# Kernel optimization log

Hardware: AMD Instinct MI355X
Metric: run time of the kernel (lower is better)

The kernel has to match this reference:

```python
import jax, jax.numpy as jnp
import numpy as np

IN_FEATURES = 1024
OUT_FEATURES = 64
DEGREE = 3
NUM_KNOTS = 10
BATCH = 8192
K0 = NUM_KNOTS + DEGREE  # number of basis columns / control points per edge


def b_spline_basis(x, knots, degree):
    """Vectorized Cox-de Boor recursion.
    x: (..., ) values in [0,1]; knots: (K0+1,).
    Returns (..., K0) basis; last `degree` columns are zero-padded (matches
    control_points width of num_knots+degree as in the original module).
    """
    t = knots
    n0 = t.shape[0] - 1  # = K0 degree-0 intervals
    xe = x[..., None]
    basis = ((xe >= t[:-1]) & (xe < t[1:])).astype(x.dtype)  # (..., K0)
    for p in range(1, degree + 1):
        ti = t[: n0 - p]
        tip = t[p:n0]
        ti1 = t[1 : n0 - p + 1]
        tip1 = t[p + 1 : n0 + 1]
        d1 = jnp.where(tip - ti > 0, tip - ti, jnp.ones_like(ti))
        d2 = jnp.where(tip1 - ti1 > 0, tip1 - ti1, jnp.ones_like(ti1))
        left = jnp.where(tip - ti > 0, (xe - ti) / d1, 0.0) * basis[..., : n0 - p]
        right = jnp.where(tip1 - ti1 > 0, (tip1 - xe) / d2, 0.0) * basis[..., 1 : n0 - p + 1]
        new = left + right
        pad = jnp.zeros(x.shape + (p,), x.dtype)
        basis = jnp.concatenate([new, pad], axis=-1)
    return basis


def setup_inputs() -> dict:
    key = jax.random.key(0)
    k1, k2 = jax.random.split(key)
    x = jax.random.uniform(k1, (BATCH, IN_FEATURES), dtype=jnp.float32)
    knots = jnp.linspace(0.0, 1.0, NUM_KNOTS + DEGREE + 1, dtype=jnp.float32)
    control_points = jax.random.normal(k2, (OUT_FEATURES, IN_FEATURES, K0), dtype=jnp.float32)
    return {"x": x, "knots": knots, "control_points": control_points}


def reference(x, knots, control_points):
    # basis: (B, in, K0) computed once per input feature (original recomputes
    # it out_features times inside a double loop -- same math, fused here).
    basis = b_spline_basis(x, knots, DEGREE)
    # outputs[b, o] = sum_j sum_k basis[b, j, k] * control_points[o, j, k]
    return jnp.einsum("bjk,ojk->bo", basis, control_points)
```

## Files before the change

kernel.cpp:

```cpp
#include <hip/hip_runtime.h>
#include <hip/hip_bf16.h>
#include <stdint.h>

#define IN_F   1024
#define OUT_F  64
#define BATCH  8192
#define BM     128
#define JSPLIT 16
#define JPB    (IN_F / JSPLIT)
#define JC     8
#define NCH    (JPB / JC)
#define BT_BYTES  (JC * 2048)
#define X_BYTES   (BM * JC * 4)
#define BUF_BYTES (BT_BYTES + X_BYTES)
#define OUTSZ  (BATCH * OUT_F)

typedef __attribute__((ext_vector_type(8)))  short short8;
typedef __attribute__((ext_vector_type(16))) float f32x16;

__global__ void kan_prep(const float* __restrict__ cp, __hip_bfloat16* __restrict__ bt) {
    int j = blockIdx.x * 4 + (threadIdx.x >> 6);
    int o = threadIdx.x & 63;
    const float* src = cp + ((size_t)o * IN_F + j) * 13;
    float v[16];
#pragma unroll
    for (int k = 0; k < 13; ++k) v[k] = src[k];
#pragma unroll
    for (int k = 13; k < 16; ++k) v[k] = 0.0f;
    __hip_bfloat16* dst = bt + (size_t)j * 1024;
#pragma unroll
    for (int kh = 0; kh < 2; ++kh)
#pragma unroll
        for (int e = 0; e < 8; ++e)
            dst[kh * 512 + o * 8 + e] = __float2bfloat16(v[kh * 8 + e]);
}

__device__ __forceinline__ uint64_t funnel64(uint64_t V, int p) {
    uint64_t r;
    if (p >= 0) r = (p >= 64) ? 0ull : (V << p);
    else { int q = -p; r = (q >= 64) ? 0ull : (V >> q); }
    return r;
}

template<bool PART>
__launch_bounds__(256, 4)
__global__ void kan_main(const float* __restrict__ x,
                         const __hip_bfloat16* __restrict__ bt,
                         float* __restrict__ outp) {
    __shared__ __attribute__((aligned(16))) char lds[2 * BUF_BYTES];

    const int tid   = threadIdx.x;
    const int w     = tid >> 6;
    const int lane  = tid & 63;
    const int l31   = lane & 31;
    const int khalf = lane >> 5;
    const int k0    = khalf << 3;

    const int r0 = blockIdx.x * BM;
    const int j0 = blockIdx.y * JPB;

    const char*  btg = (const char*)bt + (size_t)j0 * 2048;
    const float* xg  = x + (size_t)(r0 + (tid >> 1)) * IN_F + j0 + (tid & 1) * 4;

    uint4 g0, g1, g2, g3, gx;

#define LOAD(ch) do {                                            \
        const char* cb = btg + (ch) * BT_BYTES + tid * 16;       \
        g0 = *(const uint4*)(cb);                                \
        g1 = *(const uint4*)(cb + 4096);                         \
        g2 = *(const uint4*)(cb + 8192);                         \
        g3 = *(const uint4*)(cb + 12288);                        \
        gx = *(const uint4*)(xg + (ch) * JC);                    \
    } while (0)

#define WRITE(boff) do {                                         \
        char* d = lds + (boff) + tid * 16;                       \
        *(uint4*)(d)          = g0;                              \
        *(uint4*)(d + 4096)   = g1;                              \
        *(uint4*)(d + 8192)   = g2;                              \
        *(uint4*)(d + 12288)  = g3;                              \
        *(uint4*)(lds + (boff) + BT_BYTES + tid * 16) = gx;      \
    } while (0)

    f32x16 acc0, acc1;
#pragma unroll
    for (int i = 0; i < 16; ++i) { acc0[i] = 0.0f; acc1[i] = 0.0f; }

    LOAD(0);
    WRITE(0);
    LOAD(1);
    __syncthreads();

    int cur = 0;
#pragma unroll 1
    for (int ch = 0; ch < NCH; ++ch) {
        if (ch + 1 < NCH) WRITE(cur ^ BUF_BYTES);
        if (ch + 2 < NCH) LOAD(ch + 2);

        {
            const char* base = lds + cur;
            float xv[8];
            const char* xr = base + BT_BYTES + (w * 32 + l31) * 32;
            *(float4*)&xv[0] = *(const float4*)(xr);
            *(float4*)&xv[4] = *(const float4*)(xr + 16);
            const char* bbb = base + khalf * 1024 + l31 * 16;
#pragma unroll
            for (int jl = 0; jl < JC; ++jl) {
                const short8 b0 = *(const short8*)(bbb + jl * 2048);
                const short8 b1 = *(const short8*)(bbb + jl * 2048 + 512);

                const float xvv = xv[jl];
                float t  = xvv * 13.0f;
                float mf = floorf(t);
                mf = fminf(mf, 12.0f);
                float uu = t - mf;
                int   m  = (int)mf;
                float u2 = uu * uu, u3 = u2 * uu;
                float B3 = u3 * (1.0f / 6.0f);
                float omu = 1.0f - uu;
                float B0 = omu * omu * omu * (1.0f / 6.0f);
                float B1 = (0.5f * u3 - u2) + (2.0f / 3.0f);
                float B2 = 1.0f - B0 - B1 - B3;
                B3 = (m >= 10) ? 0.0f : B3;
                B2 = (m >= 11) ? 0.0f : B2;
                B1 = (m >= 12) ? 0.0f : B1;
                uint32_t P01, P23;
                asm("v_cvt_pk_bf16_f32 %0, %1, %2" : "=v"(P01) : "v"(B0), "v"(B1));
                asm("v_cvt_pk_bf16_f32 %0, %1, %2" : "=v"(P23) : "v"(B2), "v"(B3));
                uint64_t V = ((uint64_t)P23 << 32) | (uint64_t)P01;
                int p = ((m - 3 - k0) << 4);
                uint64_t flo = funnel64(V, p);
                uint64_t fhi = funnel64(V, p - 64);
                union { uint64_t q[2]; short8 s; } cv;
                cv.q[0] = flo; cv.q[1] = fhi;

                acc0 = __builtin_amdgcn_mfma_f32_32x32x16_bf16(cv.s, b0, acc0, 0, 0, 0);
                acc1 = __builtin_amdgcn_mfma_f32_32x32x16_bf16(cv.s, b1, acc1, 0, 0, 0);
            }
        }

        if (ch + 1 < NCH) __syncthreads();
        cur ^= BUF_BYTES;
    }
#undef LOAD
#undef WRITE

    float* op = PART ? (outp + (size_t)blockIdx.y * OUTSZ) : outp;
#pragma unroll
    for (int r = 0; r < 16; ++r) {
        int row = (r & 3) + 8 * (r >> 2) + 4 * khalf;
        float* po = op + (size_t)(r0 + w * 32 + row) * OUT_F;
        if (PART) {
            po[l31]      = acc0[r];
            po[l31 + 32] = acc1[r];
        } else {
            atomicAdd(po + l31,      acc0[r]);
            atomicAdd(po + l31 + 32, acc1[r]);
        }
    }
}

__global__ void kan_reduce(const float* __restrict__ part, float* __restrict__ out) {
    const int i = (blockIdx.x * 256 + threadIdx.x) * 4;
    float4 s = {0.0f, 0.0f, 0.0f, 0.0f};
#pragma unroll
    for (int b = 0; b < JSPLIT; ++b) {
        const float4 v = *(const float4*)(part + (size_t)b * OUTSZ + i);
        s.x += v.x; s.y += v.y; s.z += v.z; s.w += v.w;
    }
    *(float4*)(out + i) = s;
}

extern "C" void kernel_launch(void* const* d_in, const int* in_sizes, int n_in,
                              void* d_out, int out_size, void* d_ws, size_t ws_size,
                              hipStream_t stream) {
    const float* x  = (const float*)d_in[0];
    const float* cp = (const float*)d_in[2];
    float* out = (float*)d_out;
    __hip_bfloat16* bt = (__hip_bfloat16*)d_ws;
    float* part = (float*)((char*)d_ws + 2 * 1024 * 1024);

    const size_t need = 2u * 1024u * 1024u + (size_t)JSPLIT * OUTSZ * 4u;
    const bool use_part = ws_size >= need;

    kan_prep<<<dim3(IN_F / 4), dim3(256), 0, stream>>>(cp, bt);
    if (use_part) {
        kan_main<true><<<dim3(BATCH / BM, JSPLIT), dim3(256), 0, stream>>>(x, bt, part);
        kan_reduce<<<dim3(OUTSZ / 1024), dim3(256), 0, stream>>>(part, out);
    } else {
        hipMemsetAsync(d_out, 0, (size_t)out_size * sizeof(float), stream);
        kan_main<false><<<dim3(BATCH / BM, JSPLIT), dim3(256), 0, stream>>>(x, bt, out);
    }
}
```

Before: 49.30 us.

## Double the J-split, halve chunk size, and store bf16 partial sums

Raises the split of the input-feature dimension from 16 to 32 blocks and halves the per-chunk width to 4, with launch bounds raised to 8 blocks per CU, to get more blocks in flight and more occupancy. Partial outputs are now written as bf16 instead of fp32, which halves partial-buffer traffic, and the reduce kernel widens to 8 elements per thread with bf16-to-fp32 conversion. The cost is twice as many partial buffers for the reduce to read, shorter pipelines per block, and lower precision in the partial sums.

```diff
diff --git a/kernel.cpp b/kernel.cpp
--- a/kernel.cpp
+++ b/kernel.cpp
@@ -6,9 +6,9 @@
 #define OUT_F  64
 #define BATCH  8192
 #define BM     128
-#define JSPLIT 16
+#define JSPLIT 32
 #define JPB    (IN_F / JSPLIT)
-#define JC     8
+#define JC     4
 #define NCH    (JPB / JC)
 #define BT_BYTES  (JC * 2048)
 #define X_BYTES   (BM * JC * 4)
@@ -43,10 +43,10 @@
 }
 
 template<bool PART>
-__launch_bounds__(256, 4)
+__launch_bounds__(256, 8)
 __global__ void kan_main(const float* __restrict__ x,
                          const __hip_bfloat16* __restrict__ bt,
-                         float* __restrict__ outp) {
+                         void* __restrict__ outp) {
     __shared__ __attribute__((aligned(16))) char lds[2 * BUF_BYTES];
 
     const int tid   = threadIdx.x;
@@ -60,26 +60,23 @@
     const int j0 = blockIdx.y * JPB;
 
     const char*  btg = (const char*)bt + (size_t)j0 * 2048;
-    const float* xg  = x + (size_t)(r0 + (tid >> 1)) * IN_F + j0 + (tid & 1) * 4;
-
-    uint4 g0, g1, g2, g3, gx;
+    const float* xg  = x + (size_t)(r0 + (tid >> 1)) * IN_F + j0 + (tid & 1) * 2;
+
+    uint4  g0, g1;
+    float2 gx;
 
 #define LOAD(ch) do {                                            \
-        const char* cb = btg + (ch) * BT_BYTES + tid * 16;       \
+        const char* cb = btg + (ch) * BT_BYTES + tid * 32;       \
         g0 = *(const uint4*)(cb);                                \
-        g1 = *(const uint4*)(cb + 4096);                         \
-        g2 = *(const uint4*)(cb + 8192);                         \
-        g3 = *(const uint4*)(cb + 12288);                        \
-        gx = *(const uint4*)(xg + (ch) * JC);                    \
+        g1 = *(const uint4*)(cb + 16);                           \
+        gx = *(const float2*)(xg + (ch) * JC);                   \
     } while (0)
 
 #define WRITE(boff) do {                                         \
-        char* d = lds + (boff) + tid * 16;                       \
-        *(uint4*)(d)          = g0;                              \
-        *(uint4*)(d + 4096)   = g1;                              \
-        *(uint4*)(d + 8192)   = g2;                              \
-        *(uint4*)(d + 12288)  = g3;                              \
-        *(uint4*)(lds + (boff) + BT_BYTES + tid * 16) = gx;      \
+        char* d = lds + (boff) + tid * 32;                       \
+        *(uint4*)(d)      = g0;                                  \
+        *(uint4*)(d + 16) = g1;                                  \
+        *(float2*)(lds + (boff) + BT_BYTES + tid * 8) = gx;      \
     } while (0)
 
     f32x16 acc0, acc1;
@@ -99,10 +96,8 @@
 
         {
             const char* base = lds + cur;
-            float xv[8];
-            const char* xr = base + BT_BYTES + (w * 32 + l31) * 32;
-            *(float4*)&xv[0] = *(const float4*)(xr);
-            *(float4*)&xv[4] = *(const float4*)(xr + 16);
+            float xv[4];
+            *(float4*)&xv[0] = *(const float4*)(base + BT_BYTES + (w * 32 + l31) * 16);
             const char* bbb = base + khalf * 1024 + l31 * 16;
 #pragma unroll
             for (int jl = 0; jl < JC; ++jl) {
@@ -145,30 +140,44 @@
 #undef LOAD
 #undef WRITE
 
-    float* op = PART ? (outp + (size_t)blockIdx.y * OUTSZ) : outp;
-#pragma unroll
-    for (int r = 0; r < 16; ++r) {
-        int row = (r & 3) + 8 * (r >> 2) + 4 * khalf;
-        float* po = op + (size_t)(r0 + w * 32 + row) * OUT_F;
-        if (PART) {
-            po[l31]      = acc0[r];
-            po[l31 + 32] = acc1[r];
-        } else {
+    if (PART) {
+        __hip_bfloat16* op = (__hip_bfloat16*)outp + (size_t)blockIdx.y * OUTSZ;
+#pragma unroll
+        for (int r = 0; r < 16; ++r) {
+            int row = (r & 3) + 8 * (r >> 2) + 4 * khalf;
+            __hip_bfloat16* po = op + (size_t)(r0 + w * 32 + row) * OUT_F;
+            po[l31]      = __float2bfloat16(acc0[r]);
+            po[l31 + 32] = __float2bfloat16(acc1[r]);
+        }
+    } else {
+        float* op = (float*)outp;
+#pragma unroll
+        for (int r = 0; r < 16; ++r) {
+            int row = (r & 3) + 8 * (r >> 2) + 4 * khalf;
+            float* po = op + (size_t)(r0 + w * 32 + row) * OUT_F;
             atomicAdd(po + l31,      acc0[r]);
             atomicAdd(po + l31 + 32, acc1[r]);
         }
     }
 }
 
-__global__ void kan_reduce(const float* __restrict__ part, float* __restrict__ out) {
-    const int i = (blockIdx.x * 256 + threadIdx.x) * 4;
-    float4 s = {0.0f, 0.0f, 0.0f, 0.0f};
+__global__ void kan_reduce(const __hip_bfloat16* __restrict__ part,
+                           float* __restrict__ out) {
+    const int i = (blockIdx.x * 256 + threadIdx.x) * 8;
+    float s[8] = {0, 0, 0, 0, 0, 0, 0, 0};
 #pragma unroll
     for (int b = 0; b < JSPLIT; ++b) {
-        const float4 v = *(const float4*)(part + (size_t)b * OUTSZ + i);
-        s.x += v.x; s.y += v.y; s.z += v.z; s.w += v.w;
-    }
-    *(float4*)(out + i) = s;
+        const short8 v = *(const short8*)(part + (size_t)b * OUTSZ + i);
+#pragma unroll
+        for (int e = 0; e < 8; ++e) {
+            union { uint32_t u; float f; } c;
+            c.u = ((uint32_t)(uint16_t)v[e]) << 16;
+            s[e] += c.f;
+        }
+    }
+    float4 lo = {s[0], s[1], s[2], s[3]}, hi = {s[4], s[5], s[6], s[7]};
+    *(float4*)(out + i)     = lo;
+    *(float4*)(out + i + 4) = hi;
 }
 
 extern "C" void kernel_launch(void* const* d_in, const int* in_sizes, int n_in,
@@ -177,18 +186,18 @@
     const float* x  = (const float*)d_in[0];
     const float* cp = (const float*)d_in[2];
     float* out = (float*)d_out;
-    __hip_bfloat16* bt = (__hip_bfloat16*)d_ws;
-    float* part = (float*)((char*)d_ws + 2 * 1024 * 1024);
-
-    const size_t need = 2u * 1024u * 1024u + (size_t)JSPLIT * OUTSZ * 4u;
+    __hip_bfloat16* bt   = (__hip_bfloat16*)d_ws;
+    __hip_bfloat16* part = (__hip_bfloat16*)((char*)d_ws + 2u * 1024u * 1024u);
+
+    const size_t need = 2u * 1024u * 1024u + (size_t)JSPLIT * OUTSZ * 2u;
     const bool use_part = ws_size >= need;
 
     kan_prep<<<dim3(IN_F / 4), dim3(256), 0, stream>>>(cp, bt);
     if (use_part) {
-        kan_main<true><<<dim3(BATCH / BM, JSPLIT), dim3(256), 0, stream>>>(x, bt, part);
-        kan_reduce<<<dim3(OUTSZ / 1024), dim3(256), 0, stream>>>(part, out);
+        kan_main<true><<<dim3(BATCH / BM, JSPLIT), dim3(256), 0, stream>>>(x, bt, (void*)part);
+        kan_reduce<<<dim3(OUTSZ / 2048), dim3(256), 0, stream>>>(part, out);
     } else {
         hipMemsetAsync(d_out, 0, (size_t)out_size * sizeof(float), stream);
-        kan_main<false><<<dim3(BATCH / BM, JSPLIT), dim3(256), 0, stream>>>(x, bt, out);
-    }
-}
+        kan_main<false><<<dim3(BATCH / BM, JSPLIT), dim3(256), 0, stream>>>(x, bt, (void*)d_out);
+    }
+}
```

Result: slower. 90.13 us (+82.8%).
